# Kernel tuning notes

Hardware: AMD Instinct MI355X
Metric: run time of the kernel (lower is better)

The kernel has to match this reference:

```python
import jax, jax.numpy as jnp
import numpy as np

N = 100000   # nodes
E = 600000   # edges
G = 4096     # graphs in batch
D_IN = 73
D_E = 101
D = 128      # latent_dim
BN_EPS = 1e-5


def _bn(h, gamma, beta):
    # BatchNorm1d in training mode: batch statistics (biased variance)
    m = h.mean(axis=0)
    v = h.var(axis=0)
    return (h - m) * jax.lax.rsqrt(v + BN_EPS) * gamma + beta


def setup_inputs() -> dict:
    key = jax.random.key(0)
    ks = jax.random.split(key, 24)
    inp = {
        "x": jax.random.normal(ks[0], (N, D_IN), jnp.float32),
        "edge_attr": jax.random.normal(ks[1], (E, D_E), jnp.float32),
        "src": jax.random.randint(ks[2], (E,), 0, N, jnp.int32),
        "dst": jax.random.randint(ks[3], (E,), 0, N, jnp.int32),
        "batch": jnp.sort(jax.random.randint(ks[4], (N,), 0, G, jnp.int32)),
        # node embedding Linear(73 -> 128)
        "W_emb": jax.random.normal(ks[5], (D_IN, D), jnp.float32) / np.sqrt(D_IN),
        "b_emb": jnp.zeros((D,), jnp.float32),
    }
    k = 6
    for i in range(2):
        inp[f"We{i}"] = jax.random.normal(ks[k], (D_E, D), jnp.float32) / np.sqrt(D_E); k += 1
        inp[f"be{i}"] = jnp.zeros((D,), jnp.float32)
        inp[f"W1_{i}"] = jax.random.normal(ks[k], (D, 2 * D), jnp.float32) / np.sqrt(D); k += 1
        inp[f"b1_{i}"] = jnp.zeros((2 * D,), jnp.float32)
        inp[f"g1_{i}"] = jnp.ones((2 * D,), jnp.float32)
        inp[f"bb1_{i}"] = jnp.zeros((2 * D,), jnp.float32)
        inp[f"W2_{i}"] = jax.random.normal(ks[k], (2 * D, D), jnp.float32) / np.sqrt(2 * D); k += 1
        inp[f"b2_{i}"] = jnp.zeros((D,), jnp.float32)
        inp[f"go_{i}"] = jnp.ones((D,), jnp.float32)
        inp[f"bo_{i}"] = jnp.zeros((D,), jnp.float32)
    return inp


def _forward(x, edge_attr, src, dst, batch,
             W_emb, b_emb,
             We0, be0, W1_0, b1_0, g1_0, bb1_0, W2_0, b2_0, go_0, bo_0,
             We1, be1, W1_1, b1_1, g1_1, bb1_1, W2_1, b2_1, go_1, bo_1):
    layers = [
        (We0, be0, W1_0, b1_0, g1_0, bb1_0, W2_0, b2_0, go_0, bo_0),
        (We1, be1, W1_1, b1_1, g1_1, bb1_1, W2_1, b2_1, go_1, bo_1),
    ]
    h = x @ W_emb + b_emb  # [N, D]
    n_layers = len(layers)
    for i, (We, be, W1, b1, g1, bb1, W2, b2, go, bo) in enumerate(layers):
        e = edge_attr @ We + be                         # [E, D]
        msg = jax.nn.relu(h[src] + e)                   # gather + add + ReLU
        agg = jax.ops.segment_sum(msg, dst, num_segments=N)  # scatter-sum
        z = h + agg                                     # (1 + eps) * x_i + aggr, eps = 0
        z = jax.nn.relu(_bn(z @ W1 + b1, g1, bb1))      # MLP: Linear -> BN -> ReLU
        h = _bn(z @ W2 + b2, go, bo)                    # Linear -> outer BN
        if i != n_layers - 1:
            h = jax.nn.relu(h)
        # dropout p=0 -> identity
    # global mean pool over graphs
    sums = jax.ops.segment_sum(h, batch, num_segments=G)            # [G, D]
    counts = jax.ops.segment_sum(jnp.ones((h.shape[0],), h.dtype), batch, num_segments=G)
    return sums / jnp.maximum(counts, 1.0)[:, None]


def reference(x, edge_attr, src, dst, batch,
              W_emb, b_emb,
              We0, be0, W1_0, b1_0, g1_0, bb1_0, W2_0, b2_0, go_0, bo_0,
              We1, be1, W1_1, b1_1, g1_1, bb1_1, W2_1, b2_1, go_1, bo_1):
    return _forward(x, edge_attr, src, dst, batch, W_emb, b_emb,
                    We0, be0, W1_0, b1_0, g1_0, bb1_0, W2_0, b2_0, go_0, bo_0,
                    We1, be1, W1_1, b1_1, g1_1, bb1_1, W2_1, b2_1, go_1, bo_1)
```

## Files before the change

kernel.cpp:

```cpp
#include <hip/hip_runtime.h>
#include <cstddef>

#define NN  100000
#define NE  600000
#define NG  4096
#define DIN 73
#define DE  101
#define DD  128
#define DD2 256
#define NP  100096
#define EP  600064

typedef unsigned int uint;
typedef unsigned short ushort;
typedef __attribute__((ext_vector_type(8))) short bf16x8;
typedef __attribute__((ext_vector_type(4))) float f32x4;

__device__ __forceinline__ void fadd_atomic(float* p, float v) { unsafeAtomicAdd(p, v); }

__device__ __forceinline__ ushort f2bf(float f) {
    uint u = __float_as_uint(f);
    uint r = (u + 0x7fffu + ((u >> 16) & 1u)) >> 16;
    return (ushort)r;
}
__device__ __forceinline__ float bf2f(ushort u) { return __uint_as_float(((uint)u) << 16); }

__device__ __forceinline__ bf16x8 ld_zfrag(const float* __restrict__ p) {
    const float4 f0 = *(const float4*)p;
    const float4 f1 = *(const float4*)(p + 4);
    bf16x8 r;
    r[0] = (short)f2bf(f0.x); r[1] = (short)f2bf(f0.y);
    r[2] = (short)f2bf(f0.z); r[3] = (short)f2bf(f0.w);
    r[4] = (short)f2bf(f1.x); r[5] = (short)f2bf(f1.y);
    r[6] = (short)f2bf(f1.z); r[7] = (short)f2bf(f1.w);
    return r;
}

#define BARRIER_LDS() asm volatile("s_waitcnt lgkmcnt(0)\n\ts_barrier" ::: "memory")


__global__ void hist_kernel(const int* __restrict__ dst, int* __restrict__ deg) {
    int e = blockIdx.x * blockDim.x + threadIdx.x;
    if (e < NE) atomicAdd(&deg[dst[e]], 1);
}

__global__ __launch_bounds__(256) void scan_chunk_kernel(
    const int* __restrict__ deg, int* __restrict__ offs, int* __restrict__ csums)
{
    const int b = blockIdx.x, t = threadIdx.x;
    const int base = b * 1024 + t * 4;
    int v[4];
    #pragma unroll
    for (int i = 0; i < 4; ++i) v[i] = (base + i < NN) ? deg[base + i] : 0;
    int tsum = v[0] + v[1] + v[2] + v[3];
    const int lane = t & 63, w = t >> 6;
    int x = tsum;
    #pragma unroll
    for (int d = 1; d < 64; d <<= 1) {
        int y = __shfl_up(x, d, 64);
        if (lane >= d) x += y;
    }
    __shared__ int wsum[4];
    if (lane == 63) wsum[w] = x;
    __syncthreads();
    int woff = 0;
    for (int i = 0; i < w; ++i) woff += wsum[i];
    int run = woff + x - tsum;
    #pragma unroll
    for (int i = 0; i < 4; ++i) {
        if (base + i < NN) offs[base + i] = run;
        run += v[i];
    }
    if (t == 255) csums[b] = woff + x;
}

__global__ void scan_tops_kernel(int* __restrict__ csums, int* __restrict__ offs, int nchunks) {
    if (threadIdx.x == 0 && blockIdx.x == 0) {
        int run = 0;
        for (int i = 0; i < nchunks; ++i) { int c = csums[i]; csums[i] = run; run += c; }
        offs[NN] = run;
    }
}

__global__ void scan_add_kernel(int* __restrict__ offs, const int* __restrict__ csums) {
    int i = blockIdx.x * blockDim.x + threadIdx.x;
    if (i < NN) offs[i] += csums[i >> 10];
}

__global__ void scatter_kernel(const int* __restrict__ dst, const int* __restrict__ src,
                               const int* __restrict__ offs, int* __restrict__ cursor,
                               int* __restrict__ eperm, int* __restrict__ srcp,
                               int* __restrict__ dstp)
{
    int e = blockIdx.x * blockDim.x + threadIdx.x;
    if (e >= NE) return;
    int d = dst[e];
    int pos = offs[d] + atomicAdd(&cursor[d], 1);
    eperm[e] = pos;
    srcp[pos] = src[e];
    dstp[pos] = d;
}

__global__ void gstart_kernel(const int* __restrict__ batch, int* __restrict__ gstart) {
    int n = blockIdx.x * blockDim.x + threadIdx.x;
    if (n > NN) return;
    if (n == NN) {
        for (int g = batch[NN - 1] + 1; g <= NG; ++g) gstart[g] = NN;
        return;
    }
    int b = batch[n];
    int pb = (n == 0) ? -1 : batch[n - 1];
    for (int g = pb + 1; g <= b; ++g) gstart[g] = n;
}


__global__ __launch_bounds__(256) void cvt_ea_kernel(const float* __restrict__ ea,
                                                     const int* __restrict__ eperm,
                                                     ushort* __restrict__ eabc)
{
    const int t = threadIdx.x;
    const int r = blockIdx.x * 8 + (t >> 5);
    if (r >= NE) return;
    const int pos = eperm[r];
    const int c = (t & 31) * 4;
    ushort4 o;
    #pragma unroll
    for (int i = 0; i < 4; ++i) {
        const int col = c + i;
        float v = (col < DE) ? ea[(size_t)r * DE + col] : ((col == DE) ? 1.0f : 0.0f);
        ((ushort*)&o)[i] = f2bf(v);
    }
    *(ushort4*)&eabc[(size_t)pos * 128 + c] = o;
}

__global__ void cvt_wt_kernel(const float* __restrict__ in, ushort* __restrict__ out,
                              int Kin, int Nn, int Kp, const float* __restrict__ bias)
{
    const int n = blockIdx.x;
    for (int k = threadIdx.x; k < Kp; k += blockDim.x) {
        float v = 0.0f;
        if (k < Kin) v = in[(size_t)k * Nn + n];
        else if (k == Kin && bias) v = bias[n];
        out[(size_t)n * Kp + k] = f2bf(v);
    }
}

__global__ __launch_bounds__(256, 3) void edge_agg_kernel(
    const ushort* __restrict__ eab, const ushort* __restrict__ Wt,
    const int* __restrict__ srcp, const int* __restrict__ dstp,
    const ushort* __restrict__ hb, float* __restrict__ zf)
{
    __shared__ ushort vals[128 * 128];
    __shared__ int nd[128];
    const int tid = threadIdx.x;
    const int wid = tid >> 6;
    const int msub = wid >> 1, nsl = wid & 1;
    const int lane = tid & 63, l15 = lane & 15, grp = lane >> 4;
    const int n0 = nsl * 64;

    bf16x8 A[4][4];
    #pragma unroll
    for (int nf = 0; nf < 4; ++nf)
        #pragma unroll
        for (int kk = 0; kk < 4; ++kk)
            A[nf][kk] = *(const bf16x8*)(Wt + (size_t)(n0 + nf * 16 + l15) * 128 + kk * 32 + grp * 8);

    const int rcol = tid & 127;
    const int rh   = tid >> 7;

    const int ntiles = EP / 128;
    for (int t = blockIdx.x; t < ntiles; t += gridDim.x) {
        const int r0 = t * 128;
        const int m0 = r0 + msub * 64;
        BARRIER_LDS();
        if (tid < 128) {
            const int rr = r0 + tid;
            nd[tid] = (rr < NE) ? dstp[rr] : NN;
        }
        int sp[4];
        #pragma unroll
        for (int mf = 0; mf < 4; ++mf) {
            const int rr = m0 + mf * 16 + l15;
            sp[mf] = (rr < NE) ? srcp[rr] : 0;
        }
        ushort4 hv[4][4];
        #pragma unroll
        for (int mf = 0; mf < 4; ++mf)
            #pragma unroll
            for (int nf = 0; nf < 4; ++nf)
                hv[mf][nf] = *(const ushort4*)&hb[(size_t)sp[mf] * 128 + n0 + nf * 16 + grp * 4];
        f32x4 acc[4][4];
        #pragma unroll
        for (int i = 0; i < 4; ++i)
            #pragma unroll
            for (int j = 0; j < 4; ++j) acc[i][j] = (f32x4){0.f, 0.f, 0.f, 0.f};
        #pragma unroll
        for (int kk = 0; kk < 4; ++kk) {
            bf16x8 b[4];
            #pragma unroll
            for (int mf = 0; mf < 4; ++mf)
                b[mf] = *(const bf16x8*)(eab + (size_t)(m0 + mf * 16 + l15) * 128 + kk * 32 + grp * 8);
            #pragma unroll
            for (int mf = 0; mf < 4; ++mf)
                #pragma unroll
                for (int nf = 0; nf < 4; ++nf)
                    acc[mf][nf] = __builtin_amdgcn_mfma_f32_16x16x32_bf16(A[nf][kk], b[mf], acc[mf][nf], 0, 0, 0);
        }
        #pragma unroll
        for (int mf = 0; mf < 4; ++mf) {
            const int row = msub * 64 + mf * 16 + l15;
            const int sw = (row & 7) << 3;
            #pragma unroll
            for (int nf = 0; nf < 4; ++nf) {
                const int col = n0 + nf * 16 + grp * 4;
                ushort4 o;
                o.x = f2bf(fmaxf(acc[mf][nf][0] + bf2f(hv[mf][nf].x), 0.f));
                o.y = f2bf(fmaxf(acc[mf][nf][1] + bf2f(hv[mf][nf].y), 0.f));
                o.z = f2bf(fmaxf(acc[mf][nf][2] + bf2f(hv[mf][nf].z), 0.f));
                o.w = f2bf(fmaxf(acc[mf][nf][3] + bf2f(hv[mf][nf].w), 0.f));
                *(ushort4*)&vals[row * 128 + (col ^ sw)] = o;
            }
        }
        BARRIER_LDS();
        float accs = 0.f;
        int cur = nd[rh * 64];
        #pragma unroll
        for (int r8 = 0; r8 < 8; ++r8) {
            const int rbase = rh * 64 + r8 * 8;
            float v[8];
            #pragma unroll
            for (int j = 0; j < 8; ++j)
                v[j] = bf2f(vals[(rbase + j) * 128 + (rcol ^ (((rbase + j) & 7) << 3))]);
            #pragma unroll
            for (int j = 0; j < 8; ++j) {
                const int node = nd[rbase + j];
                if (node != cur) {
                    if (cur < NN) fadd_atomic(&zf[(size_t)cur * 128 + rcol], accs);
                    accs = 0.f; cur = node;
                }
                accs += v[j];
            }
        }
        if (cur < NN) fadd_atomic(&zf[(size_t)cur * 128 + rcol], accs);
    }
}


__global__ __launch_bounds__(256, 2) void mlp1_gemm_kernel(
    const float* __restrict__ z, const ushort* __restrict__ Wt,
    const float* __restrict__ bias, ushort* __restrict__ y)
{
    const int n0 = (threadIdx.x >> 6) * 64;
    const int lane = threadIdx.x & 63, l15 = lane & 15, grp = lane >> 4;
    bf16x8 A[4][4];
    #pragma unroll
    for (int nf = 0; nf < 4; ++nf)
        #pragma unroll
        for (int kk = 0; kk < 4; ++kk)
            A[nf][kk] = *(const bf16x8*)(Wt + (size_t)(n0 + nf * 16 + l15) * 128 + kk * 32 + grp * 8);
    float4 bv[4];
    #pragma unroll
    for (int nf = 0; nf < 4; ++nf) bv[nf] = *(const float4*)&bias[n0 + nf * 16 + grp * 4];

    const int ntiles = NP / 64;
    for (int t = blockIdx.x; t < ntiles; t += gridDim.x) {
        const int m0 = t * 64;
        f32x4 acc[4][4];
        #pragma unroll
        for (int i = 0; i < 4; ++i)
            #pragma unroll
            for (int j = 0; j < 4; ++j) acc[i][j] = (f32x4){0.f, 0.f, 0.f, 0.f};
        #pragma unroll
        for (int kk = 0; kk < 4; ++kk) {
            bf16x8 b[4];
            #pragma unroll
            for (int mf = 0; mf < 4; ++mf)
                b[mf] = ld_zfrag(z + (size_t)(m0 + mf * 16 + l15) * 128 + kk * 32 + grp * 8);
            #pragma unroll
            for (int mf = 0; mf < 4; ++mf)
                #pragma unroll
                for (int nf = 0; nf < 4; ++nf)
                    acc[mf][nf] = __builtin_amdgcn_mfma_f32_16x16x32_bf16(A[nf][kk], b[mf], acc[mf][nf], 0, 0, 0);
        }
        #pragma unroll
        for (int mf = 0; mf < 4; ++mf) {
            ushort* rp = &y[(size_t)(m0 + mf * 16 + l15) * 256 + n0];
            #pragma unroll
            for (int nf = 0; nf < 4; ++nf) {
                ushort4 o;
                o.x = f2bf(acc[mf][nf][0] + bv[nf].x);
                o.y = f2bf(acc[mf][nf][1] + bv[nf].y);
                o.z = f2bf(acc[mf][nf][2] + bv[nf].z);
                o.w = f2bf(acc[mf][nf][3] + bv[nf].w);
                *(ushort4*)&rp[nf * 16 + grp * 4] = o;
            }
        }
    }
}

__global__ __launch_bounds__(256, 2) void mlp2_gemm_kernel(
    const ushort* __restrict__ y1, const ushort* __restrict__ Wt,
    const float* __restrict__ bias, ushort* __restrict__ y2)
{
    const int wid = threadIdx.x >> 6;
    const int msub = wid >> 1, nsl = wid & 1;
    const int lane = threadIdx.x & 63, l15 = lane & 15, grp = lane >> 4;
    const int n0 = nsl * 64;
    bf16x8 A[4][8];
    #pragma unroll
    for (int nf = 0; nf < 4; ++nf)
        #pragma unroll
        for (int kk = 0; kk < 8; ++kk)
            A[nf][kk] = *(const bf16x8*)(Wt + (size_t)(n0 + nf * 16 + l15) * 256 + kk * 32 + grp * 8);
    float4 bv[4];
    #pragma unroll
    for (int nf = 0; nf < 4; ++nf) bv[nf] = *(const float4*)&bias[n0 + nf * 16 + grp * 4];

    const int ntiles = NP / 128;
    for (int t = blockIdx.x; t < ntiles; t += gridDim.x) {
        const int m0 = t * 128 + msub * 64;
        f32x4 acc[4][4];
        #pragma unroll
        for (int i = 0; i < 4; ++i)
            #pragma unroll
            for (int j = 0; j < 4; ++j) acc[i][j] = (f32x4){0.f, 0.f, 0.f, 0.f};
        #pragma unroll
        for (int kk = 0; kk < 8; ++kk) {
            bf16x8 b[4];
            #pragma unroll
            for (int mf = 0; mf < 4; ++mf)
                b[mf] = *(const bf16x8*)(y1 + (size_t)(m0 + mf * 16 + l15) * 256 + kk * 32 + grp * 8);
            #pragma unroll
            for (int mf = 0; mf < 4; ++mf)
                #pragma unroll
                for (int nf = 0; nf < 4; ++nf)
                    acc[mf][nf] = __builtin_amdgcn_mfma_f32_16x16x32_bf16(A[nf][kk], b[mf], acc[mf][nf], 0, 0, 0);
        }
        #pragma unroll
        for (int mf = 0; mf < 4; ++mf) {
            ushort* rp = &y2[(size_t)(m0 + mf * 16 + l15) * 128 + n0];
            #pragma unroll
            for (int nf = 0; nf < 4; ++nf) {
                ushort4 o;
                o.x = f2bf(acc[mf][nf][0] + bv[nf].x);
                o.y = f2bf(acc[mf][nf][1] + bv[nf].y);
                o.z = f2bf(acc[mf][nf][2] + bv[nf].z);
                o.w = f2bf(acc[mf][nf][3] + bv[nf].w);
                *(ushort4*)&rp[nf * 16 + grp * 4] = o;
            }
        }
    }
}


__global__ __launch_bounds__(128) void embed_kernel(
    const float* __restrict__ x, const float* __restrict__ W,
    const float* __restrict__ b, ushort* __restrict__ hb, float* __restrict__ zf)
{
    __shared__ float xs[4][DIN];
    const int n0 = blockIdx.x * 4;
    const int d  = threadIdx.x;
    for (int idx = d; idx < 4 * DIN; idx += 128) {
        int r = idx / DIN, c = idx - r * DIN;
        xs[r][c] = x[(size_t)n0 * DIN + idx];
    }
    __syncthreads();
    float bb = b[d];
    float a0 = bb, a1 = bb, a2 = bb, a3 = bb;
    for (int k = 0; k < DIN; ++k) {
        float w = W[k * DD + d];
        a0 = fmaf(xs[0][k], w, a0);
        a1 = fmaf(xs[1][k], w, a1);
        a2 = fmaf(xs[2][k], w, a2);
        a3 = fmaf(xs[3][k], w, a3);
    }
    ushort u0 = f2bf(a0), u1 = f2bf(a1), u2 = f2bf(a2), u3 = f2bf(a3);
    hb[(size_t)(n0 + 0) * DD + d] = u0;
    hb[(size_t)(n0 + 1) * DD + d] = u1;
    hb[(size_t)(n0 + 2) * DD + d] = u2;
    hb[(size_t)(n0 + 3) * DD + d] = u3;
    zf[(size_t)(n0 + 0) * DD + d] = bf2f(u0);
    zf[(size_t)(n0 + 1) * DD + d] = bf2f(u1);
    zf[(size_t)(n0 + 2) * DD + d] = bf2f(u2);
    zf[(size_t)(n0 + 3) * DD + d] = bf2f(u3);
}

__global__ __launch_bounds__(256) void colstats256_kernel(
    const ushort* __restrict__ y, float* __restrict__ s, float* __restrict__ q)
{
    const int t = threadIdx.x;
    const int cs = (t & 63) * 4, rg = t >> 6;
    const int r0 = blockIdx.x * 256;
    float ps0 = 0, ps1 = 0, ps2 = 0, ps3 = 0, pq0 = 0, pq1 = 0, pq2 = 0, pq3 = 0;
    for (int i = rg; i < 256; i += 4) {
        const int r = r0 + i;
        if (r >= NN) break;
        ushort4 u = *(const ushort4*)&y[(size_t)r * 256 + cs];
        float f0 = bf2f(u.x), f1 = bf2f(u.y), f2v = bf2f(u.z), f3 = bf2f(u.w);
        ps0 += f0; pq0 += f0 * f0;
        ps1 += f1; pq1 += f1 * f1;
        ps2 += f2v; pq2 += f2v * f2v;
        ps3 += f3; pq3 += f3 * f3;
    }
    __shared__ float SS[4][256], SQ[4][256];
    SS[rg][cs + 0] = ps0; SS[rg][cs + 1] = ps1; SS[rg][cs + 2] = ps2; SS[rg][cs + 3] = ps3;
    SQ[rg][cs + 0] = pq0; SQ[rg][cs + 1] = pq1; SQ[rg][cs + 2] = pq2; SQ[rg][cs + 3] = pq3;
    __syncthreads();
    if (rg == 0) {
        #pragma unroll
        for (int j = 0; j < 4; ++j) {
            const int c = cs + j;
            fadd_atomic(&s[c], SS[0][c] + SS[1][c] + SS[2][c] + SS[3][c]);
            fadd_atomic(&q[c], SQ[0][c] + SQ[1][c] + SQ[2][c] + SQ[3][c]);
        }
    }
}

__global__ __launch_bounds__(256) void colstats128b_kernel(
    const ushort* __restrict__ y, float* __restrict__ s, float* __restrict__ q)
{
    const int t = threadIdx.x;
    const int cs = (t & 31) * 4, rg = t >> 5;
    const int r0 = blockIdx.x * 256;
    float ps0 = 0, ps1 = 0, ps2 = 0, ps3 = 0, pq0 = 0, pq1 = 0, pq2 = 0, pq3 = 0;
    for (int i = rg; i < 256; i += 8) {
        const int r = r0 + i;
        if (r >= NN) break;
        ushort4 u = *(const ushort4*)&y[(size_t)r * 128 + cs];
        float f0 = bf2f(u.x), f1 = bf2f(u.y), f2v = bf2f(u.z), f3 = bf2f(u.w);
        ps0 += f0; pq0 += f0 * f0;
        ps1 += f1; pq1 += f1 * f1;
        ps2 += f2v; pq2 += f2v * f2v;
        ps3 += f3; pq3 += f3 * f3;
    }
    __shared__ float SS[8][128], SQ[8][128];
    SS[rg][cs + 0] = ps0; SS[rg][cs + 1] = ps1; SS[rg][cs + 2] = ps2; SS[rg][cs + 3] = ps3;
    SQ[rg][cs + 0] = pq0; SQ[rg][cs + 1] = pq1; SQ[rg][cs + 2] = pq2; SQ[rg][cs + 3] = pq3;
    __syncthreads();
    if (rg == 0) {
        #pragma unroll
        for (int j = 0; j < 4; ++j) {
            const int c = cs + j;
            float sv = 0, qv = 0;
            #pragma unroll
            for (int g = 0; g < 8; ++g) { sv += SS[g][c]; qv += SQ[g][c]; }
            fadd_atomic(&s[c], sv);
            fadd_atomic(&q[c], qv);
        }
    }
}

__global__ void finalize_kernel(const float* __restrict__ s, const float* __restrict__ sq,
                                const float* __restrict__ g, const float* __restrict__ bb,
                                float* __restrict__ a, float* __restrict__ c,
                                int dim, float invN)
{
    int d = blockIdx.x * blockDim.x + threadIdx.x;
    if (d >= dim) return;
    float m  = s[d] * invN;
    float v  = sq[d] * invN - m * m;
    float rs = rsqrtf(v + 1e-5f);
    float ai = g[d] * rs;
    a[d] = ai;
    c[d] = bb[d] - m * ai;
}

__global__ void bnrelu_bf_kernel(ushort* __restrict__ y, const float* __restrict__ a,
                                 const float* __restrict__ c)
{
    int i = blockIdx.x * blockDim.x + threadIdx.x;
    const int stride = gridDim.x * blockDim.x;
    for (; i < NN * 64; i += stride) {
        const int cb = (i & 63) * 4;
        ushort4 u = *(const ushort4*)&y[(size_t)i * 4];
        const float4 av = *(const float4*)&a[cb];
        const float4 cv = *(const float4*)&c[cb];
        ushort4 o;
        o.x = f2bf(fmaxf(fmaf(bf2f(u.x), av.x, cv.x), 0.f));
        o.y = f2bf(fmaxf(fmaf(bf2f(u.y), av.y, cv.y), 0.f));
        o.z = f2bf(fmaxf(fmaf(bf2f(u.z), av.z, cv.z), 0.f));
        o.w = f2bf(fmaxf(fmaf(bf2f(u.w), av.w, cv.w), 0.f));
        *(ushort4*)&y[(size_t)i * 4] = o;
    }
}

__global__ void bnrelu_hb_kernel(ushort* __restrict__ hb, const float* __restrict__ a,
                                 const float* __restrict__ c, float* __restrict__ zf)
{
    int i = blockIdx.x * blockDim.x + threadIdx.x;
    const int stride = gridDim.x * blockDim.x;
    for (; i < NN * 32; i += stride) {
        const int cb = (i & 31) * 4;
        ushort4 u = *(const ushort4*)&hb[(size_t)i * 4];
        const float4 av = *(const float4*)&a[cb];
        const float4 cv = *(const float4*)&c[cb];
        ushort4 o;
        o.x = f2bf(fmaxf(fmaf(bf2f(u.x), av.x, cv.x), 0.f));
        o.y = f2bf(fmaxf(fmaf(bf2f(u.y), av.y, cv.y), 0.f));
        o.z = f2bf(fmaxf(fmaf(bf2f(u.z), av.z, cv.z), 0.f));
        o.w = f2bf(fmaxf(fmaf(bf2f(u.w), av.w, cv.w), 0.f));
        *(ushort4*)&hb[(size_t)i * 4] = o;
        float4 zo;
        zo.x = bf2f(o.x); zo.y = bf2f(o.y); zo.z = bf2f(o.z); zo.w = bf2f(o.w);
        *(float4*)&zf[(size_t)i * 4] = zo;
    }
}

__global__ __launch_bounds__(256) void pool_kernel(
    const ushort* __restrict__ hb, const float* __restrict__ a2, const float* __restrict__ c2,
    const int* __restrict__ gstart, float* __restrict__ out)
{
    const int g = blockIdx.x * 4 + (threadIdx.x >> 6);
    if (g >= NG) return;
    const int lane = threadIdx.x & 63;
    const int s = gstart[g], t = gstart[g + 1];
    float a0 = 0.f, a1 = 0.f;
    for (int n = s; n < t; ++n) {
        const uint v = *(const uint*)&hb[(size_t)n * 128 + lane * 2];
        a0 += __uint_as_float(v << 16);
        a1 += __uint_as_float(v & 0xffff0000u);
    }
    const int d0 = lane * 2;
    float2 o;
    if (t > s) {
        const float inv = 1.0f / (float)(t - s);
        o.x = fmaf(a2[d0 + 0], a0 * inv, c2[d0 + 0]);
        o.y = fmaf(a2[d0 + 1], a1 * inv, c2[d0 + 1]);
    } else {
        o.x = 0.f; o.y = 0.f;
    }
    *(float2*)&out[(size_t)g * 128 + d0] = o;
}


extern "C" void kernel_launch(void* const* d_in, const int* in_sizes, int n_in,
                              void* d_out, int out_size, void* d_ws, size_t ws_size,
                              hipStream_t stream)
{
    (void)in_sizes; (void)n_in; (void)out_size; (void)ws_size;
    const float* x     = (const float*)d_in[0];
    const float* ea    = (const float*)d_in[1];
    const int*   src   = (const int*)d_in[2];
    const int*   dst   = (const int*)d_in[3];
    const int*   batch = (const int*)d_in[4];
    const float* W_emb = (const float*)d_in[5];
    const float* b_emb = (const float*)d_in[6];

    char* ws = (char*)d_ws;
    auto alloc = [&](size_t bytes) { void* p = ws; ws += (bytes + 255) & ~(size_t)255; return p; };

    ushort* hb   = (ushort*)alloc((size_t)NP * 128 * 2);
    float*  zf   = (float*) alloc((size_t)NP * 128 * 4);
    ushort* eabc = (ushort*)alloc((size_t)EP * 128 * 2);
    ushort* y1b  = (ushort*)alloc((size_t)NP * 256 * 2);
    int* deg    = (int*)alloc((size_t)NN * 4);
    int* offs   = (int*)alloc((size_t)(NN + 1) * 4);
    int* eperm  = (int*)alloc((size_t)NE * 4);
    int* srcp   = (int*)alloc((size_t)NE * 4);
    int* dstp   = (int*)alloc((size_t)NE * 4);
    int* csums  = (int*)alloc(128 * 4);
    int* gstart = (int*)alloc((size_t)(NG + 1) * 4);
    ushort* Wet[2], *W1t[2], *W2t[2];
    for (int l = 0; l < 2; ++l) {
        Wet[l] = (ushort*)alloc(128 * 128 * 2);
        W1t[l] = (ushort*)alloc(256 * 128 * 2);
        W2t[l] = (ushort*)alloc(128 * 256 * 2);
    }
    float* st = (float*)alloc(2048 * 4);
    float* s1 = st,        *sq1 = st + 256, *a1 = st + 512,  *c1 = st + 768;
    float* s2 = st + 1024, *sq2 = st + 1152, *a2 = st + 1280, *c2 = st + 1408;
    float* out = (float*)d_out;

    const int NCHUNK = (NN + 1023) / 1024;

    hipMemsetAsync(deg, 0, (size_t)NN * 4, stream);
    hist_kernel<<<(NE + 255) / 256, 256, 0, stream>>>(dst, deg);
    scan_chunk_kernel<<<NCHUNK, 256, 0, stream>>>(deg, offs, csums);
    scan_tops_kernel<<<1, 1, 0, stream>>>(csums, offs, NCHUNK);
    scan_add_kernel<<<(NN + 255) / 256, 256, 0, stream>>>(offs, csums);
    hipMemsetAsync(deg, 0, (size_t)NN * 4, stream);
    scatter_kernel<<<(NE + 255) / 256, 256, 0, stream>>>(dst, src, offs, deg, eperm, srcp, dstp);
    gstart_kernel<<<(NN + 256) / 256, 256, 0, stream>>>(batch, gstart);

    cvt_ea_kernel<<<(NE + 7) / 8, 256, 0, stream>>>(ea, eperm, eabc);
    for (int l = 0; l < 2; ++l) {
        const float* const* L = (const float* const*)(d_in + 7 + l * 10);
        cvt_wt_kernel<<<128, 128, 0, stream>>>(L[0], Wet[l], 101, 128, 128, L[1]);
        cvt_wt_kernel<<<256, 128, 0, stream>>>(L[2], W1t[l], 128, 256, 128, nullptr);
        cvt_wt_kernel<<<128, 128, 0, stream>>>(L[6], W2t[l], 256, 128, 256, nullptr);
    }

    embed_kernel<<<NN / 4, 128, 0, stream>>>(x, W_emb, b_emb, hb, zf);

    for (int layer = 0; layer < 2; ++layer) {
        const float* const* L = (const float* const*)(d_in + 7 + layer * 10);
        const float* b1  = L[3];
        const float* g1  = L[4]; const float* bb1 = L[5];
        const float* b2  = L[7];
        const float* go  = L[8]; const float* bo  = L[9];

        edge_agg_kernel<<<1172, 256, 0, stream>>>(eabc, Wet[layer], srcp, dstp, hb, zf);

        hipMemsetAsync(s1, 0, 512 * sizeof(float), stream);
        hipMemsetAsync(s2, 0, 256 * sizeof(float), stream);

        mlp1_gemm_kernel<<<782, 256, 0, stream>>>(zf, W1t[layer], b1, y1b);
        colstats256_kernel<<<NP / 256 + 1, 256, 0, stream>>>(y1b, s1, sq1);
        finalize_kernel<<<1, 256, 0, stream>>>(s1, sq1, g1, bb1, a1, c1, 256, 1.0f / NN);
        bnrelu_bf_kernel<<<2048, 256, 0, stream>>>(y1b, a1, c1);
        mlp2_gemm_kernel<<<391, 256, 0, stream>>>(y1b, W2t[layer], b2, hb);
        colstats128b_kernel<<<NP / 256 + 1, 256, 0, stream>>>(hb, s2, sq2);
        finalize_kernel<<<1, 128, 0, stream>>>(s2, sq2, go, bo, a2, c2, 128, 1.0f / NN);

        if (layer == 0) {
            bnrelu_hb_kernel<<<2048, 256, 0, stream>>>(hb, a2, c2, zf);
        } else {
            pool_kernel<<<NG / 4, 256, 0, stream>>>(hb, a2, c2, gstart, out);
        }
    }
}
```

Before: 1.119 ms.

## Fuse BN column statistics into MLP1 GEMM epilogue and simplify edge reduction loop

Column sum and sum-of-squares for the first BatchNorm are now accumulated in the mlp1 GEMM epilogue, with wave shuffles and atomics, instead of in a separate colstats256 pass that re-read the 100k x 256 bf16 buffer. This removes one full read of that intermediate and one kernel launch. The edge aggregation kernel also drops its launch-bounds occupancy hint from 3 to 2 blocks per CU and replaces the unrolled 8-row LDS read batch with a simple row loop. That may lower load-level parallelism but frees registers. Extra register pressure in the mlp1 epilogue (32 accumulators) could hurt occupancy there.

```diff
diff --git a/kernel.cpp b/kernel.cpp
--- a/kernel.cpp
+++ b/kernel.cpp
@@ -145,7 +145,7 @@
     }
 }
 
-__global__ __launch_bounds__(256, 3) void edge_agg_kernel(
+__global__ __launch_bounds__(256, 2) void edge_agg_kernel(
     const ushort* __restrict__ eab, const ushort* __restrict__ Wt,
     const int* __restrict__ srcp, const int* __restrict__ dstp,
     const ushort* __restrict__ hb, float* __restrict__ zf)
@@ -224,22 +224,14 @@
         BARRIER_LDS();
         float accs = 0.f;
         int cur = nd[rh * 64];
-        #pragma unroll
-        for (int r8 = 0; r8 < 8; ++r8) {
-            const int rbase = rh * 64 + r8 * 8;
-            float v[8];
-            #pragma unroll
-            for (int j = 0; j < 8; ++j)
-                v[j] = bf2f(vals[(rbase + j) * 128 + (rcol ^ (((rbase + j) & 7) << 3))]);
-            #pragma unroll
-            for (int j = 0; j < 8; ++j) {
-                const int node = nd[rbase + j];
-                if (node != cur) {
-                    if (cur < NN) fadd_atomic(&zf[(size_t)cur * 128 + rcol], accs);
-                    accs = 0.f; cur = node;
-                }
-                accs += v[j];
+        for (int r = rh * 64; r < rh * 64 + 64; ++r) {
+            const int node = nd[r];
+            const float v = bf2f(vals[r * 128 + (rcol ^ ((r & 7) << 3))]);
+            if (node != cur) {
+                if (cur < NN) fadd_atomic(&zf[(size_t)cur * 128 + rcol], accs);
+                accs = 0.f; cur = node;
             }
+            accs += v;
         }
         if (cur < NN) fadd_atomic(&zf[(size_t)cur * 128 + rcol], accs);
     }
@@ -248,7 +240,8 @@
 
 __global__ __launch_bounds__(256, 2) void mlp1_gemm_kernel(
     const float* __restrict__ z, const ushort* __restrict__ Wt,
-    const float* __restrict__ bias, ushort* __restrict__ y)
+    const float* __restrict__ bias, ushort* __restrict__ y,
+    float* __restrict__ s1, float* __restrict__ sq1)
 {
     const int n0 = (threadIdx.x >> 6) * 64;
     const int lane = threadIdx.x & 63, l15 = lane & 15, grp = lane >> 4;
@@ -261,6 +254,8 @@
     float4 bv[4];
     #pragma unroll
     for (int nf = 0; nf < 4; ++nf) bv[nf] = *(const float4*)&bias[n0 + nf * 16 + grp * 4];
+
+    float sj[4][4] = {}, qj[4][4] = {};
 
     const int ntiles = NP / 64;
     for (int t = blockIdx.x; t < ntiles; t += gridDim.x) {
@@ -284,7 +279,9 @@
         }
         #pragma unroll
         for (int mf = 0; mf < 4; ++mf) {
-            ushort* rp = &y[(size_t)(m0 + mf * 16 + l15) * 256 + n0];
+            const int m = m0 + mf * 16 + l15;
+            const bool valid = m < NN;
+            ushort* rp = &y[(size_t)m * 256 + n0];
             #pragma unroll
             for (int nf = 0; nf < 4; ++nf) {
                 ushort4 o;
@@ -293,6 +290,30 @@
                 o.z = f2bf(acc[mf][nf][2] + bv[nf].z);
                 o.w = f2bf(acc[mf][nf][3] + bv[nf].w);
                 *(ushort4*)&rp[nf * 16 + grp * 4] = o;
+                if (valid) {
+                    float v0 = bf2f(o.x), v1 = bf2f(o.y), v2 = bf2f(o.z), v3 = bf2f(o.w);
+                    sj[nf][0] += v0; qj[nf][0] += v0 * v0;
+                    sj[nf][1] += v1; qj[nf][1] += v1 * v1;
+                    sj[nf][2] += v2; qj[nf][2] += v2 * v2;
+                    sj[nf][3] += v3; qj[nf][3] += v3 * v3;
+                }
+            }
+        }
+    }
+    #pragma unroll
+    for (int nf = 0; nf < 4; ++nf) {
+        #pragma unroll
+        for (int j = 0; j < 4; ++j) {
+            float s = sj[nf][j], q = qj[nf][j];
+            #pragma unroll
+            for (int off = 1; off < 16; off <<= 1) {
+                s += __shfl_xor(s, off, 16);
+                q += __shfl_xor(q, off, 16);
+            }
+            if (l15 == 0) {
+                const int col = n0 + nf * 16 + grp * 4 + j;
+                fadd_atomic(&s1[col], s);
+                fadd_atomic(&sq1[col], q);
             }
         }
     }
@@ -383,37 +404,6 @@
     zf[(size_t)(n0 + 1) * DD + d] = bf2f(u1);
     zf[(size_t)(n0 + 2) * DD + d] = bf2f(u2);
     zf[(size_t)(n0 + 3) * DD + d] = bf2f(u3);
-}
-
-__global__ __launch_bounds__(256) void colstats256_kernel(
-    const ushort* __restrict__ y, float* __restrict__ s, float* __restrict__ q)
-{
-    const int t = threadIdx.x;
-    const int cs = (t & 63) * 4, rg = t >> 6;
-    const int r0 = blockIdx.x * 256;
-    float ps0 = 0, ps1 = 0, ps2 = 0, ps3 = 0, pq0 = 0, pq1 = 0, pq2 = 0, pq3 = 0;
-    for (int i = rg; i < 256; i += 4) {
-        const int r = r0 + i;
-        if (r >= NN) break;
-        ushort4 u = *(const ushort4*)&y[(size_t)r * 256 + cs];
-        float f0 = bf2f(u.x), f1 = bf2f(u.y), f2v = bf2f(u.z), f3 = bf2f(u.w);
-        ps0 += f0; pq0 += f0 * f0;
-        ps1 += f1; pq1 += f1 * f1;
-        ps2 += f2v; pq2 += f2v * f2v;
-        ps3 += f3; pq3 += f3 * f3;
-    }
-    __shared__ float SS[4][256], SQ[4][256];
-    SS[rg][cs + 0] = ps0; SS[rg][cs + 1] = ps1; SS[rg][cs + 2] = ps2; SS[rg][cs + 3] = ps3;
-    SQ[rg][cs + 0] = pq0; SQ[rg][cs + 1] = pq1; SQ[rg][cs + 2] = pq2; SQ[rg][cs + 3] = pq3;
-    __syncthreads();
-    if (rg == 0) {
-        #pragma unroll
-        for (int j = 0; j < 4; ++j) {
-            const int c = cs + j;
-            fadd_atomic(&s[c], SS[0][c] + SS[1][c] + SS[2][c] + SS[3][c]);
-            fadd_atomic(&q[c], SQ[0][c] + SQ[1][c] + SQ[2][c] + SQ[3][c]);
-        }
-    }
 }
 
 __global__ __launch_bounds__(256) void colstats128b_kernel(
@@ -599,13 +589,12 @@
         const float* b2  = L[7];
         const float* go  = L[8]; const float* bo  = L[9];
 
-        edge_agg_kernel<<<1172, 256, 0, stream>>>(eabc, Wet[layer], srcp, dstp, hb, zf);
-
         hipMemsetAsync(s1, 0, 512 * sizeof(float), stream);
         hipMemsetAsync(s2, 0, 256 * sizeof(float), stream);
 
-        mlp1_gemm_kernel<<<782, 256, 0, stream>>>(zf, W1t[layer], b1, y1b);
-        colstats256_kernel<<<NP / 256 + 1, 256, 0, stream>>>(y1b, s1, sq1);
+        edge_agg_kernel<<<1172, 256, 0, stream>>>(eabc, Wet[layer], srcp, dstp, hb, zf);
+
+        mlp1_gemm_kernel<<<782, 256, 0, stream>>>(zf, W1t[layer], b1, y1b, s1, sq1);
         finalize_kernel<<<1, 256, 0, stream>>>(s1, sq1, g1, bb1, a1, c1, 256, 1.0f / NN);
         bnrelu_bf_kernel<<<2048, 256, 0, stream>>>(y1b, a1, c1);
         mlp2_gemm_kernel<<<391, 256, 0, stream>>>(y1b, W2t[layer], b2, hb);
```

Measured after the change: 1.036 ms, median of 2. 7.4% less time.
